# Optimization experiments

Hardware: AMD Instinct MI355X
Metric: run time of the kernel (lower is better)

## Reference

```python
import jax, jax.numpy as jnp
import numpy as np

EMBED_DIM = 1024
NUM_HEADS = 16
NUM_GLOBAL = 4
NUM_LOCAL = NUM_HEADS - NUM_GLOBAL
WINDOW = 256
HEAD_DIM = EMBED_DIM // NUM_HEADS


def setup_inputs() -> dict:
    key = jax.random.key(0)
    k1, k2, k3 = jax.random.split(key, 3)
    B, S = 4, 2048
    x = jax.random.normal(k1, (B, S, EMBED_DIM), dtype=jnp.float32)
    w_qkv = jax.random.normal(k2, (EMBED_DIM, 3 * EMBED_DIM), dtype=jnp.float32) * (EMBED_DIM ** -0.5)
    b_qkv = jnp.zeros((3 * EMBED_DIM,), dtype=jnp.float32)
    w_out = jax.random.normal(k3, (EMBED_DIM, EMBED_DIM), dtype=jnp.float32) * (EMBED_DIM ** -0.5)
    b_out = jnp.zeros((EMBED_DIM,), dtype=jnp.float32)
    return {"x": x, "w_qkv": w_qkv, "b_qkv": b_qkv, "w_out": w_out, "b_out": b_out}


def _masks(seq_len):
    i = jnp.arange(seq_len)[:, None]
    j = jnp.arange(seq_len)[None, :]
    diff = i - j
    global_mask = diff < 0                      # True = masked (strictly future)
    local_mask = (diff < 0) | (diff > WINDOW)   # True = masked (outside window)
    return global_mask, local_mask


def _attend(q, k, v, mask):
    # q,k,v: [B,h,S,D]; mask: [S,S] True = disallow
    scores = jnp.einsum('bhqd,bhkd->bhqk', q, k) * (HEAD_DIM ** -0.5)
    scores = jnp.where(mask[None, None], -jnp.inf, scores)
    w = jax.nn.softmax(scores, axis=-1)
    return jnp.einsum('bhqk,bhkd->bhqd', w, v)


def reference(x, w_qkv, b_qkv, w_out, b_out):
    B, S, _ = x.shape
    qkv = x @ w_qkv + b_qkv                      # [B,S,3E]
    q, k, v = jnp.split(qkv, 3, axis=-1)
    def heads(t):
        return t.reshape(B, S, NUM_HEADS, HEAD_DIM).transpose(0, 2, 1, 3)
    q, k, v = heads(q), heads(k), heads(v)       # [B,H,S,D]
    gmask, lmask = _masks(S)
    ctx_g = _attend(q[:, :NUM_GLOBAL], k[:, :NUM_GLOBAL], v[:, :NUM_GLOBAL], gmask)
    ctx_l = _attend(q[:, NUM_GLOBAL:], k[:, NUM_GLOBAL:], v[:, NUM_GLOBAL:], lmask)
    ctx = jnp.concatenate([ctx_g, ctx_l], axis=1)          # [B,H,S,D]
    ctx = ctx.transpose(0, 2, 1, 3).reshape(B, S, EMBED_DIM)
    return ctx @ w_out + b_out
```

## Files before the change

kernel.cpp:

```cpp
#include <hip/hip_runtime.h>
#include <stdint.h>

#define EMB 1024
#define SEQ 2048
#define NB 4
#define NH 16
#define HD 64
#define NGLOB 4
#define WIN 256
#define MTOT (NB*SEQ)
#define NQKV (3*EMB)

#define PART_U16 2176
#define JOBS_PER_BG 260

typedef __attribute__((ext_vector_type(8))) short bf16x8;
typedef __attribute__((ext_vector_type(4))) float f32x4;
typedef __attribute__((ext_vector_type(16))) float f32x16;
typedef unsigned short u16;
typedef unsigned int u32;

#define CL2 0.18033688011112042f

#if __has_builtin(__builtin_amdgcn_exp2f)
#define EXP2(x) __builtin_amdgcn_exp2f(x)
#else
#define EXP2(x) exp2f(x)
#endif

__device__ __forceinline__ u16 f2bf(float f) {
  u32 u = __builtin_bit_cast(u32, f);
  u += 0x7fffu + ((u >> 16) & 1u);
  return (u16)(u >> 16);
}

__device__ __forceinline__ float bf2f(u16 v) {
  u32 u = (u32)v << 16;
  return __builtin_bit_cast(float, u);
}

__device__ __forceinline__ u32 packtrunc(float a, float b) {
  u32 ua = __builtin_bit_cast(u32, a);
  u32 ub = __builtin_bit_cast(u32, b);
  return (ua >> 16) | (ub & 0xffff0000u);
}


#define MFMA16(a, b, c) __builtin_amdgcn_mfma_f32_16x16x32_bf16(a, b, c, 0, 0, 0)
#define MFMA32(a, b, c) __builtin_amdgcn_mfma_f32_32x32x16_bf16(a, b, c, 0, 0, 0)
#define GLD16(g, l) __builtin_amdgcn_global_load_lds( \
    (const __attribute__((address_space(1))) void*)(g), \
    (__attribute__((address_space(3))) void*)(l), 16, 0, 0)

__global__ void k_cast(const float* __restrict__ in, u16* __restrict__ out, int n4) {
  int i = blockIdx.x * blockDim.x + threadIdx.x;
  if (i >= n4) return;
  float4 f = ((const float4*)in)[i];
  ushort4 o;
  o.x = f2bf(f.x); o.y = f2bf(f.y); o.z = f2bf(f.z); o.w = f2bf(f.w);
  ((ushort4*)out)[i] = o;
}

__global__ void k_transpose_cast(const float* __restrict__ w, u16* __restrict__ wt,
                                 int R, int C) {
  __shared__ float tile[32][33];
  int c0 = blockIdx.x * 32, r0 = blockIdx.y * 32;
  int tx = threadIdx.x, ty = threadIdx.y;
  #pragma unroll
  for (int j = 0; j < 32; j += 8)
    tile[ty + j][tx] = w[(size_t)(r0 + ty + j) * C + (c0 + tx)];
  __syncthreads();
  #pragma unroll
  for (int j = 0; j < 32; j += 8)
    wt[(size_t)(c0 + ty + j) * R + (r0 + tx)] = f2bf(tile[tx][ty + j]);
}

template <int EPI>
__global__ __launch_bounds__(256, 2) void k_gemm(
    const u16* __restrict__ A, const u16* __restrict__ Bt,
    const float* __restrict__ bias,
    u16* __restrict__ Qo, u16* __restrict__ Ko, u16* __restrict__ Vt,
    float* __restrict__ outp) {
  __shared__ __align__(16) u16 ldsA[128 * 64];
  __shared__ __align__(16) u16 ldsB[128 * 64];
  const int tid = threadIdx.x;
  const int w = tid >> 6, lane = tid & 63;
  const int wm = w >> 1, wn = w & 1;
  const int m0 = blockIdx.x * 128, n0 = blockIdx.y * 128;
  const int rq = lane & 15, g = lane >> 4;

  const int srow = lane >> 3;
  const int scol = ((lane & 7) ^ srow) << 3;

  f32x4 acc[4][4] = {};
  char* ldsAb = (char*)ldsA;
  char* ldsBb = (char*)ldsB;

  for (int k0 = 0; k0 < EMB; k0 += 64) {
    #pragma unroll
    for (int it = 0; it < 4; ++it) {
      int t = w * 4 + it;
      int row = t * 8 + srow;
      GLD16(A + (size_t)(m0 + row) * EMB + k0 + scol, ldsAb + t * 1024);
      GLD16(Bt + (size_t)(n0 + row) * EMB + k0 + scol, ldsBb + t * 1024);
    }
    __syncthreads();
    #pragma unroll
    for (int ks = 0; ks < 2; ++ks) {
      bf16x8 af[4], bfr[4];
      #pragma unroll
      for (int i = 0; i < 4; ++i) {
        int rowA = wm * 64 + i * 16 + rq;
        int off = (ks * 64 + (g << 4)) ^ ((rowA & 7) << 4);
        af[i] = *(const bf16x8*)(ldsAb + rowA * 128 + off);
        int rowB = wn * 64 + i * 16 + rq;
        int offb = (ks * 64 + (g << 4)) ^ ((rowB & 7) << 4);
        bfr[i] = *(const bf16x8*)(ldsBb + rowB * 128 + offb);
      }
      #pragma unroll
      for (int mi = 0; mi < 4; ++mi)
        #pragma unroll
        for (int ni = 0; ni < 4; ++ni)
          acc[mi][ni] = MFMA16(af[mi], bfr[ni], acc[mi][ni]);
    }
    __syncthreads();
  }

  #pragma unroll
  for (int ni = 0; ni < 4; ++ni) {
    int col = n0 + wn * 64 + ni * 16 + rq;
    float bv = bias[col];
    if (EPI == 0) {
      int part = col >> 10;
      int hh = (col & 1023) >> 6;
      int d = col & 63;
      #pragma unroll
      for (int mi = 0; mi < 4; ++mi) {
        #pragma unroll
        for (int i = 0; i < 4; ++i) {
          int m = m0 + wm * 64 + mi * 16 + g * 4 + i;
          int b = m >> 11, s = m & 2047;
          u16 val = f2bf(acc[mi][ni][i] + bv);
          size_t bh = (size_t)(b * NH + hh);
          if (part == 0)      Qo[(bh * SEQ + s) * HD + d] = val;
          else if (part == 1) Ko[(bh * SEQ + s) * HD + d] = val;
          else                Vt[((bh * 128 + (s >> 4)) * 64 + d) * 16 + (s & 15)] = val;
        }
      }
    } else {
      #pragma unroll
      for (int mi = 0; mi < 4; ++mi)
        #pragma unroll
        for (int i = 0; i < 4; ++i) {
          int m = m0 + wm * 64 + mi * 16 + g * 4 + i;
          outp[(size_t)m * EMB + col] = acc[mi][ni][i] + bv;
        }
    }
  }
}

__global__ __launch_bounds__(256, 4) void k_attn(
    const u16* __restrict__ Q, const u16* __restrict__ K,
    const u16* __restrict__ Vt, u16* __restrict__ ctx,
    u16* __restrict__ part) {
  const int w = threadIdx.x >> 6, lane = threadIdx.x & 63;
  const int l31 = lane & 31;
  const int hi = lane >> 5;
  const bool hib = hi != 0;
  const int hi8 = hi * 8, hi4 = hi * 4;

  const int gid = blockIdx.x;
  const int x = gid & 7;
  const int jb = gid >> 3;
  const bool isglob = jb < 130;

  int bh, qt, cstart, clen, band = 0, slot = 0;
  if (isglob) {
    int pk = jb * 4 + w;
    int bg = 2 * x + (pk >= JOBS_PER_BG);
    int r = (pk >= JOBS_PER_BG) ? pk - JOBS_PER_BG : pk;
    int b = 0;
    while (b < 7 && r >= 9 * (b + 1) * (b + 2) / 2) ++b;
    band = b;
    int rb = r - 9 * b * (b + 1) / 2;
    int nseg = b + 1;
    if (b == 7) nseg = 8;
    int qoff = rb / nseg;
    int seg = rb - qoff * nseg;
    qt = 9 * b + qoff;
    bh = (bg >> 2) * 16 + (bg & 3);
    slot = bg * JOBS_PER_BG + r;
    int L = qt + 1;
    int base = L / nseg, rm = L - base * nseg;
    clen = base + (seg < rm ? 1 : 0);
    cstart = seg * base + (seg < rm ? seg : rm);
  } else {
    int lj = (jb - 130) * 4 + w;
    int bls = lj >> 6;
    int bl = 6 * x + bls;
    qt = lj & 63;
    bh = (bl / 12) * 16 + 4 + (bl % 12);
    int qb_ = qt * 32;
    int klo = (qb_ > WIN) ? qb_ - WIN : 0;
    cstart = klo >> 5;
    clen = qt + 1 - cstart;
  }

  const int qb = qt * 32;
  const int h = bh & 15;
  const int b_ = bh >> 4;
  const bool isloc = !isglob;

  const u16* Qp = Q + (size_t)bh * SEQ * HD;
  const u16* Kp = K + (size_t)bh * SEQ * HD;
  const u16* Vp = Vt + (size_t)bh * SEQ * HD;

  const int q = qb + l31;
  const float NINF = -__builtin_inff();

  bf16x8 qf[4];
  #pragma unroll
  for (int jj = 0; jj < 4; ++jj)
    qf[jj] = *(const bf16x8*)(Qp + (size_t)q * HD + jj * 16 + hi8);

  f32x16 oacc[2] = {};
  float m = NINF;
  float l = 0.f;

  int kc = cstart * 32;
  #pragma unroll 2
  for (int it = 0; it < clen; ++it, kc += 32) {
    bf16x8 kf0, kf1, kf2, kf3, vf[2][2];
    {
      const u16* Kr = Kp + (size_t)(kc + l31) * HD + hi8;
      kf0 = *(const bf16x8*)(Kr);
      kf1 = *(const bf16x8*)(Kr + 16);
      kf2 = *(const bf16x8*)(Kr + 32);
      kf3 = *(const bf16x8*)(Kr + 48);
      const u16* Vb = Vp + (size_t)(kc >> 4) * 1024 + hi8;
      #pragma unroll
      for (int dt = 0; dt < 2; ++dt)
        #pragma unroll
        for (int sl = 0; sl < 2; ++sl)
          vf[dt][sl] = *(const bf16x8*)(Vb + (sl * 64 + dt * 32 + l31) * 16);
    }

    f32x16 s0 = {}, s1 = {};
    s0 = MFMA32(kf0, qf[0], s0);
    s1 = MFMA32(kf2, qf[2], s1);
    s0 = MFMA32(kf1, qf[1], s0);
    s1 = MFMA32(kf3, qf[3], s1);

    const bool needs_mask = (kc == qb) || (isloc && (qb - kc > 225));
    float p[16];
    float cmax = NINF;
    if (needs_mask) {
      #pragma unroll
      for (int r = 0; r < 16; ++r) {
        int key = kc + hi4 + (r & 3) + 8 * (r >> 2);
        float v = s0[r] + s1[r];
        bool bad = (key > q) || (isloc && (q - key > WIN));
        p[r] = bad ? NINF : v;
        cmax = fmaxf(cmax, p[r]);
      }
    } else {
      #pragma unroll
      for (int r = 0; r < 16; ++r) {
        p[r] = s0[r] + s1[r];
        cmax = fmaxf(cmax, p[r]);
      }
    }
    cmax = fmaxf(cmax, __shfl_xor(cmax, 32));

    float muC;
    if (__any(cmax > m + 64.f)) {
      float mn = fmaxf(m, cmax);
      muC = (mn == NINF) ? 0.f : mn * CL2;
      float oldC = (m == NINF) ? muC : m * CL2;
      float f = EXP2(oldC - muC);
      m = mn;
      l *= f;
      #pragma unroll
      for (int dt = 0; dt < 2; ++dt)
        #pragma unroll
        for (int r = 0; r < 16; ++r)
          oacc[dt][r] *= f;
    } else {
      muC = (m == NINF) ? 0.f : m * CL2;
    }

    float psum = 0.f;
    #pragma unroll
    for (int r = 0; r < 16; ++r) {
      float e = EXP2(__builtin_fmaf(p[r], CL2, -muC));
      p[r] = e;
      psum += e;
    }
    psum += __shfl_xor(psum, 32);
    l += psum;

    union { u32 u[4]; bf16x8 v; } pbf[2];
    #pragma unroll
    for (int sl = 0; sl < 2; ++sl) {
      int s8 = sl * 8;
      u32 X0 = packtrunc(p[s8 + 0], p[s8 + 1]);
      u32 X1 = packtrunc(p[s8 + 2], p[s8 + 3]);
      u32 X2 = packtrunc(p[s8 + 4], p[s8 + 5]);
      u32 X3 = packtrunc(p[s8 + 6], p[s8 + 7]);
      u32 oX0 = (u32)__shfl_xor((int)X0, 32);
      u32 oX1 = (u32)__shfl_xor((int)X1, 32);
      u32 oX2 = (u32)__shfl_xor((int)X2, 32);
      u32 oX3 = (u32)__shfl_xor((int)X3, 32);
      pbf[sl].u[0] = hib ? oX2 : X0;
      pbf[sl].u[1] = hib ? oX3 : X1;
      pbf[sl].u[2] = hib ? X2 : oX0;
      pbf[sl].u[3] = hib ? X3 : oX1;
    }

    #pragma unroll
    for (int dt = 0; dt < 2; ++dt)
      #pragma unroll
      for (int sl = 0; sl < 2; ++sl)
        oacc[dt] = MFMA32(vf[dt][sl], pbf[sl].v, oacc[dt]);
  }

  if (isglob && band != 0) {
    u16* PB = part + (size_t)slot * PART_U16;
    #pragma unroll
    for (int dt = 0; dt < 2; ++dt)
      #pragma unroll
      for (int r = 0; r < 16; ++r) {
        int d = dt * 32 + hi4 + (r & 3) + 8 * (r >> 2);
        PB[d * 32 + l31] = f2bf(oacc[dt][r]);
      }
    float* PF = (float*)(PB + 2048);
    if (hi == 0) { PF[l31] = m; PF[32 + l31] = l; }
  } else {
    float linv = 1.f / l;
    #pragma unroll
    for (int dt = 0; dt < 2; ++dt) {
      #pragma unroll
      for (int r = 0; r < 16; ++r) {
        int d = dt * 32 + hi4 + (r & 3) + 8 * (r >> 2);
        int e = h * HD + d;
        ctx[(size_t)(b_ * SEQ + q) * EMB + e] = f2bf(oacc[dt][r] * linv);
      }
    }
  }
}

__global__ __launch_bounds__(256, 4) void k_merge(
    const u16* __restrict__ part, u16* __restrict__ ctx) {
  const int t = blockIdx.x;
  const int bg = t & 15;
  const int qt = t >> 4;
  const int band = qt / 9;
  const int nseg = band + 1;
  if (nseg == 1) return;
  const int jbase = bg * JOBS_PER_BG + 9 * band * (band + 1) / 2
                    + (qt - 9 * band) * nseg;
  const int bh = (bg >> 2) * 16 + (bg & 3);
  const int qb = qt * 32;
  const int h = bh & 15;
  const int bb = bh >> 4;

  __shared__ u16 ob[64][34];
  __shared__ float fml[8][64];

  const int tid = threadIdx.x;
  for (int e = tid; e < nseg * 64; e += 256) {
    int s = e >> 6, k = e & 63;
    fml[s][k] = ((const float*)(part + (size_t)(jbase + s) * PART_U16 + 2048))[k];
  }
  __syncthreads();

  const int dd = tid & 63;
  const int qg = tid >> 6;
  float M[8], Lsum[8], val[8];
  #pragma unroll
  for (int i = 0; i < 8; ++i) {
    int qq = qg * 8 + i;
    float mx = fml[0][qq];
    for (int s = 1; s < nseg; ++s) mx = fmaxf(mx, fml[s][qq]);
    M[i] = mx; Lsum[i] = 0.f; val[i] = 0.f;
  }

  for (int s = 0; s < nseg; ++s) {
    __syncthreads();
    const u32* src = (const u32*)(part + (size_t)(jbase + s) * PART_U16);
    #pragma unroll
    for (int c = 0; c < 4; ++c) {
      int wd = tid * 4 + c;
      *(u32*)&ob[wd >> 4][(wd & 15) * 2] = src[wd];
    }
    __syncthreads();
    #pragma unroll
    for (int i = 0; i < 8; ++i) {
      int qq = qg * 8 + i;
      float wgt = EXP2((fml[s][qq] - M[i]) * CL2);
      Lsum[i] += wgt * fml[s][32 + qq];
      val[i] += wgt * bf2f(ob[dd][qq]);
    }
  }

  #pragma unroll
  for (int i = 0; i < 8; ++i) {
    int qq = qg * 8 + i;
    ctx[(size_t)(bb * SEQ + (qb + qq)) * EMB + h * HD + dd] = f2bf(val[i] / Lsum[i]);
  }
}

extern "C" void kernel_launch(void* const* d_in, const int* in_sizes, int n_in,
                              void* d_out, int out_size, void* d_ws, size_t ws_size,
                              hipStream_t stream) {
  const float* x     = (const float*)d_in[0];
  const float* w_qkv = (const float*)d_in[1];
  const float* b_qkv = (const float*)d_in[2];
  const float* w_out = (const float*)d_in[3];
  const float* b_out = (const float*)d_in[4];
  float* out = (float*)d_out;

  char* ws = (char*)d_ws;
  u16* xb    = (u16*)(ws);
  u16* wqkvT = (u16*)(ws + (16ull << 20));
  u16* woutT = (u16*)(ws + (22ull << 20));
  u16* Qb    = (u16*)(ws + (24ull << 20));
  u16* Kb    = (u16*)(ws + (40ull << 20));
  u16* Vt    = (u16*)(ws + (56ull << 20));
  u16* ctx   = (u16*)(ws + (72ull << 20));
  u16* part  = xb;

  k_cast<<<(MTOT * EMB / 4) / 256, 256, 0, stream>>>(x, xb, MTOT * EMB / 4);
  dim3 tb(32, 8);
  k_transpose_cast<<<dim3(NQKV / 32, EMB / 32), tb, 0, stream>>>(w_qkv, wqkvT, EMB, NQKV);
  k_transpose_cast<<<dim3(EMB / 32, EMB / 32), tb, 0, stream>>>(w_out, woutT, EMB, EMB);

  k_gemm<0><<<dim3(MTOT / 128, NQKV / 128), 256, 0, stream>>>(
      xb, wqkvT, b_qkv, Qb, Kb, Vt, nullptr);

  k_attn<<<dim3(226 * 8), 256, 0, stream>>>(Qb, Kb, Vt, ctx, part);
  k_merge<<<dim3(1024), 256, 0, stream>>>(part, ctx);

  k_gemm<1><<<dim3(MTOT / 128, EMB / 128), 256, 0, stream>>>(
      ctx, woutT, b_out, nullptr, nullptr, nullptr, out);
}
```

Measured before the change: 197.1 us.

## Transpose attention MFMA output layout for coalesced ctx stores and simplify merge

Swaps the MFMA operands in the P·V product so the accumulator holds query rows by register and head-dim columns by lane. Per-query rescale factors and 1/l are then fetched with lane shuffles. Context and partial-result stores become contiguous along the head dimension instead of strided 2-byte scatters across rows. The merge kernel drops its shared-memory staging and barriers and reads the partials directly with coalesced loads, at the cost of some redundant global reads of the m/l stats.

```diff
diff --git a/kernel.cpp b/kernel.cpp
--- a/kernel.cpp
+++ b/kernel.cpp
@@ -281,10 +281,11 @@
       m = mn;
       l *= f;
       #pragma unroll
-      for (int dt = 0; dt < 2; ++dt)
-        #pragma unroll
-        for (int r = 0; r < 16; ++r)
-          oacc[dt][r] *= f;
+      for (int r = 0; r < 16; ++r) {
+        float fq = __shfl(f, (r & 3) + 8 * (r >> 2) + 4 * hi);
+        oacc[0][r] *= fq;
+        oacc[1][r] *= fq;
+      }
     } else {
       muC = (m == NINF) ? 0.f : m * CL2;
     }
@@ -321,7 +322,7 @@
     for (int dt = 0; dt < 2; ++dt)
       #pragma unroll
       for (int sl = 0; sl < 2; ++sl)
-        oacc[dt] = MFMA32(vf[dt][sl], pbf[sl].v, oacc[dt]);
+        oacc[dt] = MFMA32(pbf[sl].v, vf[dt][sl], oacc[dt]);
   }
 
   if (isglob && band != 0) {
@@ -330,8 +331,8 @@
     for (int dt = 0; dt < 2; ++dt)
       #pragma unroll
       for (int r = 0; r < 16; ++r) {
-        int d = dt * 32 + hi4 + (r & 3) + 8 * (r >> 2);
-        PB[d * 32 + l31] = f2bf(oacc[dt][r]);
+        int qoff = (r & 3) + 8 * (r >> 2) + 4 * hi;
+        PB[qoff * 64 + dt * 32 + l31] = f2bf(oacc[dt][r]);
       }
     float* PF = (float*)(PB + 2048);
     if (hi == 0) { PF[l31] = m; PF[32 + l31] = l; }
@@ -341,9 +342,10 @@
     for (int dt = 0; dt < 2; ++dt) {
       #pragma unroll
       for (int r = 0; r < 16; ++r) {
-        int d = dt * 32 + hi4 + (r & 3) + 8 * (r >> 2);
-        int e = h * HD + d;
-        ctx[(size_t)(b_ * SEQ + q) * EMB + e] = f2bf(oacc[dt][r] * linv);
+        int qoff = (r & 3) + 8 * (r >> 2) + 4 * hi;
+        float lq = __shfl(linv, qoff);
+        ctx[(size_t)(b_ * SEQ + qb + qoff) * EMB + h * HD + dt * 32 + l31] =
+            f2bf(oacc[dt][r] * lq);
       }
     }
   }
@@ -355,8 +357,8 @@
   const int bg = t & 15;
   const int qt = t >> 4;
   const int band = qt / 9;
-  const int nseg = band + 1;
-  if (nseg == 1) return;
+  const int nseg = (band == 7) ? 8 : band + 1;
+  if (band == 0) return;
   const int jbase = bg * JOBS_PER_BG + 9 * band * (band + 1) / 2
                     + (qt - 9 * band) * nseg;
   const int bh = (bg >> 2) * 16 + (bg & 3);
@@ -364,49 +366,26 @@
   const int h = bh & 15;
   const int bb = bh >> 4;
 
-  __shared__ u16 ob[64][34];
-  __shared__ float fml[8][64];
-
   const int tid = threadIdx.x;
-  for (int e = tid; e < nseg * 64; e += 256) {
-    int s = e >> 6, k = e & 63;
-    fml[s][k] = ((const float*)(part + (size_t)(jbase + s) * PART_U16 + 2048))[k];
-  }
-  __syncthreads();
-
   const int dd = tid & 63;
   const int qg = tid >> 6;
-  float M[8], Lsum[8], val[8];
   #pragma unroll
   for (int i = 0; i < 8; ++i) {
     int qq = qg * 8 + i;
-    float mx = fml[0][qq];
-    for (int s = 1; s < nseg; ++s) mx = fmaxf(mx, fml[s][qq]);
-    M[i] = mx; Lsum[i] = 0.f; val[i] = 0.f;
-  }
-
-  for (int s = 0; s < nseg; ++s) {
-    __syncthreads();
-    const u32* src = (const u32*)(part + (size_t)(jbase + s) * PART_U16);
-    #pragma unroll
-    for (int c = 0; c < 4; ++c) {
-      int wd = tid * 4 + c;
-      *(u32*)&ob[wd >> 4][(wd & 15) * 2] = src[wd];
-    }
-    __syncthreads();
-    #pragma unroll
-    for (int i = 0; i < 8; ++i) {
-      int qq = qg * 8 + i;
-      float wgt = EXP2((fml[s][qq] - M[i]) * CL2);
-      Lsum[i] += wgt * fml[s][32 + qq];
-      val[i] += wgt * bf2f(ob[dd][qq]);
-    }
-  }
-
-  #pragma unroll
-  for (int i = 0; i < 8; ++i) {
-    int qq = qg * 8 + i;
-    ctx[(size_t)(bb * SEQ + (qb + qq)) * EMB + h * HD + dd] = f2bf(val[i] / Lsum[i]);
+    float M = -__builtin_inff();
+    for (int s = 0; s < nseg; ++s) {
+      const float* F = (const float*)(part + (size_t)(jbase + s) * PART_U16 + 2048);
+      M = fmaxf(M, F[qq]);
+    }
+    float L = 0.f, val = 0.f;
+    for (int s = 0; s < nseg; ++s) {
+      const u16* P = part + (size_t)(jbase + s) * PART_U16;
+      const float* F = (const float*)(P + 2048);
+      float wgt = EXP2((F[qq] - M) * CL2);
+      L += wgt * F[32 + qq];
+      val += wgt * bf2f(P[qq * 64 + dd]);
+    }
+    ctx[(size_t)(bb * SEQ + (qb + qq)) * EMB + h * HD + dd] = f2bf(val / L);
   }
 }
 
```

Result: slower. 217.5 us (+10.4%).
